# Kernel optimization log

Hardware: AMD Instinct MI355X
Metric: run time of the kernel (lower is better)

Reference implementation:

```python
import jax, jax.numpy as jnp
import numpy as np

H, W, L = 80, 80, 21
NUM_ITERATIONS = 5
ALPHA, BETA, GAMMA = 160.0, 3.0, 3.0  # DenseCRFParams defaults
EPS = 1e-8


def _gaussian_kernel(feats):
    # feats: [N, d] -> K_ij = exp(-0.5 * ||f_i - f_j||^2), symmetric
    sq = jnp.sum(feats * feats, axis=1)
    d2 = sq[:, None] + sq[None, :] - 2.0 * (feats @ feats.T)
    return jnp.exp(-0.5 * jnp.maximum(d2, 0.0))


def _build_filters(image):
    # image: [3, H, W], values in [0, 255]. Lattice features are constants
    # w.r.t. autodiff in the original (custom Function), so stop_gradient.
    img = jax.lax.stop_gradient(image)
    ys, xs = jnp.meshgrid(jnp.arange(H, dtype=jnp.float32),
                          jnp.arange(W, dtype=jnp.float32), indexing="ij")
    pos = jnp.stack([xs.ravel(), ys.ravel()], axis=1)          # [N, 2]
    K_sp = _gaussian_kernel(pos / GAMMA)                        # [N, N]
    rgb = img.reshape(3, -1).T                                  # [N, 3]
    K_bi = _gaussian_kernel(jnp.concatenate([pos / ALPHA, rgb / BETA], axis=1))
    # AbstractFilter normalization: divide by filter applied to all-ones
    norm_sp = 1.0 / (K_sp.sum(axis=1) + EPS)                    # [N]
    norm_bi = 1.0 / (K_bi.sum(axis=1) + EPS)
    return K_sp, norm_sp, K_bi, norm_bi


def setup_inputs() -> dict:
    key = jax.random.key(0)
    k1, k2 = jax.random.split(key)
    image = jax.random.uniform(k1, (1, 3, H, W), dtype=jnp.float32) * 255.0
    logits = jax.random.normal(k2, (1, L, H, W), dtype=jnp.float32)
    eye = jnp.eye(L, dtype=jnp.float32)
    return {
        "image": image,
        "logits": logits,
        "spatial_ker_weights": 3.0 * eye,    # spatial_ker_weight * I
        "bilateral_ker_weights": 5.0 * eye,  # bilateral_ker_weight * I
        "compatibility_matrix": eye,
    }


def reference(image, logits, spatial_ker_weights, bilateral_ker_weights,
              compatibility_matrix):
    img = image[0]          # [3, H, W]
    unary = logits[0].reshape(L, -1)  # [L, N]
    K_sp, norm_sp, K_bi, norm_bi = _build_filters(img)
    cur = unary
    for _ in range(NUM_ITERATIONS):
        q = jax.nn.softmax(cur, axis=0)                  # [L, N]
        # K symmetric: (q @ K)[l, i] = sum_j K_ij q[l, j]
        spatial_out = spatial_ker_weights @ ((q @ K_sp) * norm_sp)
        bilateral_out = bilateral_ker_weights @ ((q @ K_bi) * norm_bi)
        msg = compatibility_matrix @ (spatial_out + bilateral_out)
        cur = msg + unary
    return cur.reshape(1, L, H, W)
```

## Files before the change

kernel.cpp:

```cpp
#include <hip/hip_runtime.h>
#include <hip/hip_bf16.h>
#include <math.h>

#define HH 80
#define WW 80
#define NPIX 6400
#define LL 21
#define NITER 5
#define C_LOG2E 1.44269504088896f

#define SJ  320
#define CHK (SJ / 32)
#define QROW 164
#define QROWS 22
#define NBLK 1000
#define NBY  20
#define NLP  11
#define SPWORK (LL * NPIX)

#define PXB 16
#define SYB (NPIX / PXB)
#define SYT 384

typedef short short8 __attribute__((ext_vector_type(8)));
typedef float f32x16 __attribute__((ext_vector_type(16)));

__device__ inline ushort bf_rne(float x) {
    uint u = __float_as_uint(x);
    return (ushort)((u + 0x7FFFu + ((u >> 16) & 1u)) >> 16);
}
__device__ inline float bf_to_f(ushort h) { return __uint_as_float(((uint)h) << 16); }
__device__ inline uint pk2(float a, float b) {
    __hip_bfloat162 t = __float22bfloat162_rn(make_float2(a, b));
    return *reinterpret_cast<uint*>(&t);
}
__device__ inline uint pk2z(float a, float b) {
    return __builtin_amdgcn_perm(__float_as_uint(b), __float_as_uint(a), 0x07060302u);
}
__device__ inline float fexp2(float x) { return __builtin_amdgcn_exp2f(x); }

__global__ void k_setup(const float* __restrict__ img, const float* __restrict__ unary,
                        const float* __restrict__ Wsp, const float* __restrict__ Wbi,
                        const float* __restrict__ C, ushort* __restrict__ fjg,
                        uint* __restrict__ fig, float* __restrict__ mhs,
                        float* __restrict__ nsp, ushort* __restrict__ qb16,
                        float* __restrict__ M1, float* __restrict__ M2) {
    int tid = threadIdx.x;
    if (blockIdx.x == 25) {
        for (int t = tid; t < LL * LL; t += 256) {
            int l = t / LL, k = t % LL;
            float a = 0.f, b = 0.f;
            for (int m = 0; m < LL; m++) {
                a += C[l * LL + m] * Wsp[m * LL + k];
                b += C[l * LL + m] * Wbi[m * LL + k];
            }
            M1[t] = a; M2[t] = b;
        }
        return;
    }
    __shared__ float sxT[WW];
    if (tid < WW) {
        float s = 0.f;
        for (int t = 0; t < WW; t++) { float d = (float)(tid - t); s += __expf(-d * d * (1.0f / 18.0f)); }
        sxT[tid] = s;
    }
    __syncthreads();
    int i = blockIdx.x * 256 + tid;
    int x = i % WW, y = i / WW;
    float f[5];
    f[0] = (float)x * (1.0f / 160.0f);
    f[1] = (float)y * (1.0f / 160.0f);
    f[2] = (img[0 * NPIX + i] - 127.5f) * (1.0f / 3.0f);
    f[3] = (img[1 * NPIX + i] - 127.5f) * (1.0f / 3.0f);
    f[4] = (img[2 * NPIX + i] - 127.5f) * (1.0f / 3.0f);
    float s = 0.f;
    ushort hi[5], lo[5], Hi[5], Lo[5];
#pragma unroll
    for (int c = 0; c < 5; c++) {
        s += f[c] * f[c];
        hi[c] = bf_rne(f[c]);
        lo[c] = bf_rne(f[c] - bf_to_f(hi[c]));
        float a = C_LOG2E * f[c];
        Hi[c] = bf_rne(a);
        Lo[c] = bf_rne(a - bf_to_f(Hi[c]));
    }
    float mi = -0.5f * C_LOG2E * s;
    mhs[i] = mi;
    ushort mih = bf_rne(mi);
    ushort mil = bf_rne(mi - bf_to_f(mih));
    {
        ushort r0[16] = { hi[0], hi[1], hi[2], hi[3], hi[4], lo[2], lo[3], lo[4],
                          hi[2], hi[3], hi[4], lo[2], lo[3], lo[4], 0x3F80, 0x3F80 };
        uint4 w0, w1;
        w0.x = (uint)r0[0] | ((uint)r0[1] << 16);  w0.y = (uint)r0[2] | ((uint)r0[3] << 16);
        w0.z = (uint)r0[4] | ((uint)r0[5] << 16);  w0.w = (uint)r0[6] | ((uint)r0[7] << 16);
        w1.x = (uint)r0[8] | ((uint)r0[9] << 16);  w1.y = (uint)r0[10] | ((uint)r0[11] << 16);
        w1.z = (uint)r0[12] | ((uint)r0[13] << 16); w1.w = (uint)r0[14] | ((uint)r0[15] << 16);
        *(uint4*)(fjg + (size_t)i * 16) = w0;
        *(uint4*)(fjg + (size_t)i * 16 + 8) = w1;
    }
    {
        ushort r1[16] = { Hi[0], Hi[1], Hi[2], Hi[3], Hi[4], Hi[2], Hi[3], Hi[4],
                          Lo[2], Lo[3], Lo[4], Lo[2], Lo[3], Lo[4], mih, mil };
        uint4 w0, w1;
        w0.x = (uint)r1[0] | ((uint)r1[1] << 16);  w0.y = (uint)r1[2] | ((uint)r1[3] << 16);
        w0.z = (uint)r1[4] | ((uint)r1[5] << 16);  w0.w = (uint)r1[6] | ((uint)r1[7] << 16);
        w1.x = (uint)r1[8] | ((uint)r1[9] << 16);  w1.y = (uint)r1[10] | ((uint)r1[11] << 16);
        w1.z = (uint)r1[12] | ((uint)r1[13] << 16); w1.w = (uint)r1[14] | ((uint)r1[15] << 16);
        *(uint4*)(fig + (size_t)i * 8) = w0;
        *(uint4*)(fig + (size_t)i * 8 + 4) = w1;
    }
    nsp[i] = 1.0f / (sxT[x] * sxT[y] + 1e-8f);
    float v[LL];
    float mx = -1e30f;
    for (int l = 0; l < LL; l++) { v[l] = unary[l * NPIX + i]; mx = fmaxf(mx, v[l]); }
    float ss = 0.f;
    for (int l = 0; l < LL; l++) { v[l] = __expf(v[l] - mx); ss += v[l]; }
    float r = 1.0f / ss;
    for (int l = 0; l < LL; l++) qb16[(size_t)l * NPIX + i] = bf_rne(v[l] * r);
}

__device__ inline f32x16 ldmhs(const float* p, int h) {
    float4 a0 = *(const float4*)(p + 8 * h);
    float4 a1 = *(const float4*)(p + 8 * h + 4);
    float4 a2 = *(const float4*)(p + 16 + 8 * h);
    float4 a3 = *(const float4*)(p + 16 + 8 * h + 4);
    f32x16 cv;
    cv[0] = a0.x;  cv[1] = a0.y;  cv[2] = a0.z;  cv[3] = a0.w;
    cv[4] = a1.x;  cv[5] = a1.y;  cv[6] = a1.z;  cv[7] = a1.w;
    cv[8] = a2.x;  cv[9] = a2.y;  cv[10] = a2.z; cv[11] = a2.w;
    cv[12] = a3.x; cv[13] = a3.y; cv[14] = a3.z; cv[15] = a3.w;
    return cv;
}

__global__ __launch_bounds__(256, 4)
void k_iter1(const float* __restrict__ mhs, const ushort* __restrict__ fjg,
             const uint* __restrict__ fig, const ushort* __restrict__ qb16,
             uint* __restrict__ bip, float* __restrict__ tmpx) {
    __shared__ __align__(16) uint  FjL[SJ * 12];
    __shared__ __align__(16) float mhsL[SJ];
    __shared__ __align__(16) uint  QL[QROWS * QROW];
    __shared__ float gT[WW];
    int tid = threadIdx.x;
    int bid = blockIdx.x;
    int bx = bid % 50, by = bid / 50;
    int j0 = by * SJ;
    for (int idx = tid; idx < QROWS * (SJ / 2); idx += 256) {
        int l = idx / (SJ / 2), jp = idx % (SJ / 2);
        uint v;
        if (l < LL) {
            const uint* p = (const uint*)qb16 + (((size_t)l * NPIX + j0) >> 1);
            v = p[jp];
        } else {
            v = 0x3F803F80u;
        }
        QL[l * QROW + jp] = v;
    }
    for (int idx = tid; idx < SJ * 2; idx += 256) {
        int r = idx >> 1, hf = idx & 1;
        uint4 v = ((const uint4*)(fjg + (size_t)(j0 + r) * 16))[hf];
        *(uint4*)&FjL[r * 12 + hf * 4] = v;
    }
    for (int idx = tid; idx < SJ; idx += 256) mhsL[idx] = mhs[j0 + idx];
    if (tid < WW) gT[tid] = __expf(-(float)(tid * tid) * (1.0f / 18.0f));
    int lane = tid & 63, wid = tid >> 6;
    int h = lane >> 5, m = lane & 31;
    int i = bx * 128 + wid * 32 + m;
    union U8 { uint u[4]; short8 s; };
    U8 bfr;
    {
        uint4 bv = *(const uint4*)(fig + (size_t)i * 8 + h * 4);
        bfr.u[0] = bv.x; bfr.u[1] = bv.y; bfr.u[2] = bv.z; bfr.u[3] = bv.w;
    }
    int jrow = (m & ~12) | ((m & 4) << 1) | ((m & 8) >> 1);
    int qrow = (m < QROWS) ? m : 0;
    __syncthreads();
    f32x16 acc;
#pragma unroll
    for (int k = 0; k < 16; k++) acc[k] = 0.f;
    const uint* qbase = &QL[qrow * QROW + h * 4];
    for (int c = 0; c < CHK; c++) {
        int jb = c * 32;
        f32x16 cv = ldmhs(&mhsL[jb], h);
        short8 af = *(const short8*)&FjL[(jb + jrow) * 12 + h * 4];
        f32x16 d1 = __builtin_amdgcn_mfma_f32_32x32x16_bf16(af, bfr.s, cv, 0, 0, 0);
        short8 qa = *(const short8*)(qbase + c * 16);
        short8 qb = *(const short8*)(qbase + c * 16 + 8);
        U8 ea;
        ea.u[0] = pk2z(fexp2(d1[0]), fexp2(d1[1]));
        ea.u[1] = pk2z(fexp2(d1[2]), fexp2(d1[3]));
        ea.u[2] = pk2z(fexp2(d1[4]), fexp2(d1[5]));
        ea.u[3] = pk2z(fexp2(d1[6]), fexp2(d1[7]));
        acc = __builtin_amdgcn_mfma_f32_32x32x16_bf16(qa, ea.s, acc, 0, 0, 0);
        U8 eb;
        eb.u[0] = pk2z(fexp2(d1[8]),  fexp2(d1[9]));
        eb.u[1] = pk2z(fexp2(d1[10]), fexp2(d1[11]));
        eb.u[2] = pk2z(fexp2(d1[12]), fexp2(d1[13]));
        eb.u[3] = pk2z(fexp2(d1[14]), fexp2(d1[15]));
        acc = __builtin_amdgcn_mfma_f32_32x32x16_bf16(qb, eb.s, acc, 0, 0, 0);
    }
#pragma unroll
    for (int r = 0; r < 16; r += 2) {
        int l = (r & 3) + 8 * (r >> 2) + 4 * h;
        if (l < LL + 1)
            bip[((size_t)by * NLP + (l >> 1)) * NPIX + i] = pk2(acc[r], acc[r + 1]);
    }
    {
        int start = (int)(((long)bid * SPWORK) / NBLK);
        int end   = (int)(((long)(bid + 1) * SPWORK) / NBLK);
        int cnt = end - start;
        if (tid < cnt) {
            int fidx = start + tid;
            int l = fidx / NPIX;
            int p = fidx - l * NPIX;
            int x = p % WW, y = p / WW;
            const ushort* rowq = qb16 + (size_t)l * NPIX + y * WW;
            float s = 0.f;
            for (int xp = 0; xp < WW; xp++) {
                int d = x - xp; d = d < 0 ? -d : d;
                s += gT[d] * bf_to_f(rowq[xp]);
            }
            tmpx[(size_t)l * NPIX + p] = s;
        }
    }
}

__global__ __launch_bounds__(SYT)
void k_syc(const float* __restrict__ unary, const float* __restrict__ tmpx,
           const uint* __restrict__ bip, const float* __restrict__ nsp,
           const float* __restrict__ M1, const float* __restrict__ M2,
           ushort* __restrict__ qb16, float* __restrict__ out, int last) {
    __shared__ float m1s[LL * 24];
    __shared__ float m2s[LL * 24];
    __shared__ float gT[HH];
    __shared__ float svL[PXB][QROWS];
    __shared__ float bvL[PXB][QROWS];
    __shared__ float aex[PXB][QROWS];
    int tid = threadIdx.x;
    int px0 = blockIdx.x * PXB;
    for (int t = tid; t < LL * LL; t += SYT) {
        int l = t / LL, k = t % LL;
        m1s[l * 24 + k] = M1[t];
        m2s[l * 24 + k] = M2[t];
    }
    if (tid < HH) gT[tid] = __expf(-(float)(tid * tid) * (1.0f / 18.0f));
    __syncthreads();
    if (tid < PXB * LL) {
        int pxl = tid & (PXB - 1);
        int l = tid >> 4;
        int px = px0 + pxl;
        int x = px % WW, y = px / WW;
        const float* base = tmpx + (size_t)l * NPIX + x;
        float s1 = 0.f;
        for (int yp = 0; yp < HH; yp++) {
            int d = y - yp; d = d < 0 ? -d : d;
            s1 += gT[d] * base[yp * WW];
        }
        svL[pxl][l] = s1;
    }
    if (tid < PXB * NLP) {
        int pxl = tid & (PXB - 1);
        int lp = tid >> 4;
        int px = px0 + pxl;
        float sa = 0.f, sb = 0.f;
        const uint* p = bip + (size_t)lp * NPIX + px;
#pragma unroll
        for (int byi = 0; byi < NBY; byi++) {
            uint v = p[(size_t)byi * NLP * NPIX];
            sa += __uint_as_float(v << 16);
            sb += __uint_as_float(v & 0xFFFF0000u);
        }
        bvL[pxl][2 * lp] = sa;
        bvL[pxl][2 * lp + 1] = sb;
    }
    __syncthreads();
    if (tid < PXB * LL) {
        int pxl = tid & (PXB - 1);
        int l = tid >> 4;
        int px = px0 + pxl;
        float ns = nsp[px];
        float nb = 1.0f / (bvL[pxl][LL] + 1e-8f);
        float s1 = 0.f, s2 = 0.f;
        const float* r1 = &m1s[l * 24];
        const float* r2 = &m2s[l * 24];
#pragma unroll
        for (int k = 0; k < LL; k++) {
            s1 = fmaf(r1[k], svL[pxl][k], s1);
            s2 = fmaf(r2[k], bvL[pxl][k], s2);
        }
        float a = unary[l * NPIX + px] + ns * s1 + nb * s2;
        if (last) out[(size_t)l * NPIX + px] = a;
        else      aex[pxl][l] = a;
    }
    if (last) return;
    __syncthreads();
    if (tid < PXB) {
        int px = px0 + tid;
        float mx = -1e30f;
        for (int l = 0; l < LL; l++) mx = fmaxf(mx, aex[tid][l]);
        float s = 0.f;
        float e[LL];
        for (int l = 0; l < LL; l++) { e[l] = __expf(aex[tid][l] - mx); s += e[l]; }
        float r = 1.0f / s;
        for (int l = 0; l < LL; l++)
            qb16[(size_t)l * NPIX + px] = bf_rne(e[l] * r);
    }
}

extern "C" void kernel_launch(void* const* d_in, const int* in_sizes, int n_in,
                              void* d_out, int out_size, void* d_ws, size_t ws_size,
                              hipStream_t stream) {
    const float* img   = (const float*)d_in[0];
    const float* unary = (const float*)d_in[1];
    const float* Wsp   = (const float*)d_in[2];
    const float* Wbi   = (const float*)d_in[3];
    const float* C     = (const float*)d_in[4];
    float* out = (float*)d_out;

    const int LN = LL * NPIX;
    float* w = (float*)d_ws;
    float*  tmpx = w;  w += LN;
    uint*   bip  = (uint*)w;    w += NBY * NLP * NPIX;
    float*  mhs  = w;  w += NPIX;
    float*  nsp  = w;  w += NPIX;
    ushort* fjg  = (ushort*)w;  w += 8 * NPIX;
    uint*   fig  = (uint*)w;    w += 8 * NPIX;
    ushort* qb16 = (ushort*)w;  w += (LN + 1) / 2;
    float*  M1   = w;  w += LL * LL;
    float*  M2   = w;  w += LL * LL;

    k_setup<<<26, 256, 0, stream>>>(img, unary, Wsp, Wbi, C, fjg, fig, mhs, nsp,
                                    qb16, M1, M2);
    for (int it = 0; it < NITER; it++) {
        int last = (it == NITER - 1);
        k_iter1<<<NBLK, 256, 0, stream>>>(mhs, fjg, fig, qb16, bip, tmpx);
        k_syc<<<SYB, SYT, 0, stream>>>(unary, tmpx, bip, nsp, M1, M2, qb16, out, last);
    }
}
```

Before: 190.2 us.

## Move self-norm term into MFMA features, add per-i term in registers, bf16 tmpx

The j-side squared-norm term is now folded into the bf16 feature vectors fed to the MFMA (swapping the ones and norm columns between fjg and fig). The i-side term is added per element in registers before exp2, which removes the shared mhs tile and the per-chunk C-operand loads, and occupancy is raised to 5 waves. The spatial x-pass intermediate is stored as bf16 and read as packed pairs, halving its traffic. The changes add extra VALU adds per exponent and a bf16 rounding of the intermediate.

```diff
diff --git a/kernel.cpp b/kernel.cpp
--- a/kernel.cpp
+++ b/kernel.cpp
@@ -86,11 +86,11 @@
     }
     float mi = -0.5f * C_LOG2E * s;
     mhs[i] = mi;
-    ushort mih = bf_rne(mi);
-    ushort mil = bf_rne(mi - bf_to_f(mih));
+    ushort mjh = bf_rne(mi);
+    ushort mjl = bf_rne(mi - bf_to_f(mjh));
     {
         ushort r0[16] = { hi[0], hi[1], hi[2], hi[3], hi[4], lo[2], lo[3], lo[4],
-                          hi[2], hi[3], hi[4], lo[2], lo[3], lo[4], 0x3F80, 0x3F80 };
+                          hi[2], hi[3], hi[4], lo[2], lo[3], lo[4], mjh, mjl };
         uint4 w0, w1;
         w0.x = (uint)r0[0] | ((uint)r0[1] << 16);  w0.y = (uint)r0[2] | ((uint)r0[3] << 16);
         w0.z = (uint)r0[4] | ((uint)r0[5] << 16);  w0.w = (uint)r0[6] | ((uint)r0[7] << 16);
@@ -101,7 +101,7 @@
     }
     {
         ushort r1[16] = { Hi[0], Hi[1], Hi[2], Hi[3], Hi[4], Hi[2], Hi[3], Hi[4],
-                          Lo[2], Lo[3], Lo[4], Lo[2], Lo[3], Lo[4], mih, mil };
+                          Lo[2], Lo[3], Lo[4], Lo[2], Lo[3], Lo[4], 0x3F80, 0x3F80 };
         uint4 w0, w1;
         w0.x = (uint)r1[0] | ((uint)r1[1] << 16);  w0.y = (uint)r1[2] | ((uint)r1[3] << 16);
         w0.z = (uint)r1[4] | ((uint)r1[5] << 16);  w0.w = (uint)r1[6] | ((uint)r1[7] << 16);
@@ -120,25 +120,11 @@
     for (int l = 0; l < LL; l++) qb16[(size_t)l * NPIX + i] = bf_rne(v[l] * r);
 }
 
-__device__ inline f32x16 ldmhs(const float* p, int h) {
-    float4 a0 = *(const float4*)(p + 8 * h);
-    float4 a1 = *(const float4*)(p + 8 * h + 4);
-    float4 a2 = *(const float4*)(p + 16 + 8 * h);
-    float4 a3 = *(const float4*)(p + 16 + 8 * h + 4);
-    f32x16 cv;
-    cv[0] = a0.x;  cv[1] = a0.y;  cv[2] = a0.z;  cv[3] = a0.w;
-    cv[4] = a1.x;  cv[5] = a1.y;  cv[6] = a1.z;  cv[7] = a1.w;
-    cv[8] = a2.x;  cv[9] = a2.y;  cv[10] = a2.z; cv[11] = a2.w;
-    cv[12] = a3.x; cv[13] = a3.y; cv[14] = a3.z; cv[15] = a3.w;
-    return cv;
-}
-
-__global__ __launch_bounds__(256, 4)
+__global__ __launch_bounds__(256, 5)
 void k_iter1(const float* __restrict__ mhs, const ushort* __restrict__ fjg,
              const uint* __restrict__ fig, const ushort* __restrict__ qb16,
-             uint* __restrict__ bip, float* __restrict__ tmpx) {
+             uint* __restrict__ bip, ushort* __restrict__ tmpx) {
     __shared__ __align__(16) uint  FjL[SJ * 12];
-    __shared__ __align__(16) float mhsL[SJ];
     __shared__ __align__(16) uint  QL[QROWS * QROW];
     __shared__ float gT[WW];
     int tid = threadIdx.x;
@@ -161,7 +147,6 @@
         uint4 v = ((const uint4*)(fjg + (size_t)(j0 + r) * 16))[hf];
         *(uint4*)&FjL[r * 12 + hf * 4] = v;
     }
-    for (int idx = tid; idx < SJ; idx += 256) mhsL[idx] = mhs[j0 + idx];
     if (tid < WW) gT[tid] = __expf(-(float)(tid * tid) * (1.0f / 18.0f));
     int lane = tid & 63, wid = tid >> 6;
     int h = lane >> 5, m = lane & 31;
@@ -172,31 +157,31 @@
         uint4 bv = *(const uint4*)(fig + (size_t)i * 8 + h * 4);
         bfr.u[0] = bv.x; bfr.u[1] = bv.y; bfr.u[2] = bv.z; bfr.u[3] = bv.w;
     }
+    float mi = mhs[i];
     int jrow = (m & ~12) | ((m & 4) << 1) | ((m & 8) >> 1);
     int qrow = (m < QROWS) ? m : 0;
     __syncthreads();
-    f32x16 acc;
-#pragma unroll
-    for (int k = 0; k < 16; k++) acc[k] = 0.f;
+    f32x16 acc, zc;
+#pragma unroll
+    for (int k = 0; k < 16; k++) { acc[k] = 0.f; zc[k] = 0.f; }
     const uint* qbase = &QL[qrow * QROW + h * 4];
     for (int c = 0; c < CHK; c++) {
         int jb = c * 32;
-        f32x16 cv = ldmhs(&mhsL[jb], h);
         short8 af = *(const short8*)&FjL[(jb + jrow) * 12 + h * 4];
-        f32x16 d1 = __builtin_amdgcn_mfma_f32_32x32x16_bf16(af, bfr.s, cv, 0, 0, 0);
+        f32x16 d1 = __builtin_amdgcn_mfma_f32_32x32x16_bf16(af, bfr.s, zc, 0, 0, 0);
         short8 qa = *(const short8*)(qbase + c * 16);
         short8 qb = *(const short8*)(qbase + c * 16 + 8);
         U8 ea;
-        ea.u[0] = pk2z(fexp2(d1[0]), fexp2(d1[1]));
-        ea.u[1] = pk2z(fexp2(d1[2]), fexp2(d1[3]));
-        ea.u[2] = pk2z(fexp2(d1[4]), fexp2(d1[5]));
-        ea.u[3] = pk2z(fexp2(d1[6]), fexp2(d1[7]));
+        ea.u[0] = pk2z(fexp2(d1[0] + mi), fexp2(d1[1] + mi));
+        ea.u[1] = pk2z(fexp2(d1[2] + mi), fexp2(d1[3] + mi));
+        ea.u[2] = pk2z(fexp2(d1[4] + mi), fexp2(d1[5] + mi));
+        ea.u[3] = pk2z(fexp2(d1[6] + mi), fexp2(d1[7] + mi));
         acc = __builtin_amdgcn_mfma_f32_32x32x16_bf16(qa, ea.s, acc, 0, 0, 0);
         U8 eb;
-        eb.u[0] = pk2z(fexp2(d1[8]),  fexp2(d1[9]));
-        eb.u[1] = pk2z(fexp2(d1[10]), fexp2(d1[11]));
-        eb.u[2] = pk2z(fexp2(d1[12]), fexp2(d1[13]));
-        eb.u[3] = pk2z(fexp2(d1[14]), fexp2(d1[15]));
+        eb.u[0] = pk2z(fexp2(d1[8]  + mi), fexp2(d1[9]  + mi));
+        eb.u[1] = pk2z(fexp2(d1[10] + mi), fexp2(d1[11] + mi));
+        eb.u[2] = pk2z(fexp2(d1[12] + mi), fexp2(d1[13] + mi));
+        eb.u[3] = pk2z(fexp2(d1[14] + mi), fexp2(d1[15] + mi));
         acc = __builtin_amdgcn_mfma_f32_32x32x16_bf16(qb, eb.s, acc, 0, 0, 0);
     }
 #pragma unroll
@@ -214,19 +199,22 @@
             int l = fidx / NPIX;
             int p = fidx - l * NPIX;
             int x = p % WW, y = p / WW;
-            const ushort* rowq = qb16 + (size_t)l * NPIX + y * WW;
+            const uint* rowq = (const uint*)(qb16 + (size_t)l * NPIX + y * WW);
             float s = 0.f;
-            for (int xp = 0; xp < WW; xp++) {
-                int d = x - xp; d = d < 0 ? -d : d;
-                s += gT[d] * bf_to_f(rowq[xp]);
+            for (int k = 0; k < WW / 2; k++) {
+                uint v = rowq[k];
+                int d0 = x - 2 * k;     d0 = d0 < 0 ? -d0 : d0;
+                int d1 = x - 2 * k - 1; d1 = d1 < 0 ? -d1 : d1;
+                s += gT[d0] * __uint_as_float(v << 16);
+                s += gT[d1] * __uint_as_float(v & 0xFFFF0000u);
             }
-            tmpx[(size_t)l * NPIX + p] = s;
+            tmpx[(size_t)l * NPIX + p] = bf_rne(s);
         }
     }
 }
 
 __global__ __launch_bounds__(SYT)
-void k_syc(const float* __restrict__ unary, const float* __restrict__ tmpx,
+void k_syc(const float* __restrict__ unary, const ushort* __restrict__ tmpx,
            const uint* __restrict__ bip, const float* __restrict__ nsp,
            const float* __restrict__ M1, const float* __restrict__ M2,
            ushort* __restrict__ qb16, float* __restrict__ out, int last) {
@@ -250,11 +238,11 @@
         int l = tid >> 4;
         int px = px0 + pxl;
         int x = px % WW, y = px / WW;
-        const float* base = tmpx + (size_t)l * NPIX + x;
+        const ushort* base = tmpx + (size_t)l * NPIX + x;
         float s1 = 0.f;
         for (int yp = 0; yp < HH; yp++) {
             int d = y - yp; d = d < 0 ? -d : d;
-            s1 += gT[d] * base[yp * WW];
+            s1 += gT[d] * bf_to_f(base[yp * WW]);
         }
         svL[pxl][l] = s1;
     }
@@ -319,7 +307,7 @@
 
     const int LN = LL * NPIX;
     float* w = (float*)d_ws;
-    float*  tmpx = w;  w += LN;
+    ushort* tmpx = (ushort*)w;  w += (LN + 1) / 2;
     uint*   bip  = (uint*)w;    w += NBY * NLP * NPIX;
     float*  mhs  = w;  w += NPIX;
     float*  nsp  = w;  w += NPIX;
```

Result: no change. 192.4 us (+1.1%).
